# Kernel optimization log

Measured on AMD Instinct MI355X. Metric: run time of the kernel, lower is better.

## Reference

```python
import jax, jax.numpy as jnp
import numpy as np

B_PARAM = 1.0
BAND_WIDTH = 0.5
LOSS_WEIGHT = 1.0
EPS_REL = 1e-5
EPS_NORM = 1e-12


def setup_inputs() -> dict:
    key = jax.random.key(0)
    k1, k2 = jax.random.split(key)
    images = jax.random.normal(k1, (1, 256, 96, 96), dtype=jnp.float32)
    gt = jax.random.normal(k2, (1, 256, 96, 96), dtype=jnp.float32)
    return {"images": images, "gt": gt}


def _cosine_raw_distance(i_feat, t_feat):
    # _create_using_dot_p: center both by mean of t over (n, h, w), L2-normalize
    # along channels, then pairwise dot products -> cosine distance in [0, 1].
    mean_t = jnp.mean(t_feat, axis=(0, 2, 3), keepdims=True)
    i_c = i_feat - mean_t
    t_c = t_feat - mean_t
    i_n = i_c / jnp.maximum(jnp.sqrt(jnp.sum(i_c * i_c, axis=1, keepdims=True)), EPS_NORM)
    t_n = t_c / jnp.maximum(jnp.sqrt(jnp.sum(t_c * t_c, axis=1, keepdims=True)), EPS_NORM)
    n, c, h, w = i_n.shape
    t_v = t_n.reshape(n, c, h * w)
    # dot[n, h, w, s] = sum_c i_n[n,c,h,w] * t_v[n,c,s]   (the conv2d 1x1 kernel trick)
    dot = jnp.einsum('nchw,ncs->nhws', i_n, t_v)
    dist = jnp.clip((1.0 - dot) / 2.0, 0.0, None)
    return dist  # [n, h, w, h*w]


def _cx_loss(i_feat, t_feat):
    raw = _cosine_raw_distance(i_feat, t_feat)                      # [n,h,w,s]
    # relative distance (Eq. 2): divide each row by its min over target positions
    rel = raw / (jnp.min(raw, axis=-1, keepdims=True) + EPS_REL)
    w = jnp.exp((B_PARAM - rel) / BAND_WIDTH)
    cx = w / jnp.sum(w, axis=-1, keepdims=True)                     # row softmax-like
    max_gt_sim = jnp.max(cx, axis=(1, 2))                           # [n, s]
    cs = jnp.mean(max_gt_sim, axis=1)                               # [n]
    loss = jnp.mean(-jnp.log(cs))
    return loss * LOSS_WEIGHT


def reference(images, gt):
    # use_vgg=False, crop_quarter=False, h*w <= max_1d_size**2 -> direct CX loss.
    return _cx_loss(images, gt)
```

## Files before the change

kernel.cpp:

```cpp
#include <hip/hip_runtime.h>
#include <hip/hip_bf16.h>

#define S 9216
#define C 256
#define NCT 12
#define NG  (NCT*8)
#define SCH 1152

typedef __bf16 bf16x8 __attribute__((ext_vector_type(8)));
typedef float f32x4 __attribute__((ext_vector_type(4)));
typedef unsigned short us8 __attribute__((ext_vector_type(8)));
typedef unsigned short us4 __attribute__((ext_vector_type(4)));

#define GLOAD_LDS16(g, l) __builtin_amdgcn_global_load_lds( \
    (const __attribute__((address_space(1))) void*)(g),     \
    (__attribute__((address_space(3))) void*)(l), 16, 0, 0)

#define A2C 2.8853900817779268f

__device__ __forceinline__ float bf2f(unsigned short u) {
    return __uint_as_float(((unsigned)u) << 16);
}
__device__ __forceinline__ unsigned short f2bfbits(float x) {
    __hip_bfloat16 h = __float2bfloat16(x);
    return *reinterpret_cast<unsigned short*>(&h);
}

__global__ __launch_bounds__(256) void k_mean(const float* __restrict__ gt,
                                              float* __restrict__ meanT) {
    const int c = blockIdx.x;
    const float* p = gt + (size_t)c * S;
    float s = 0.f;
    for (int i = threadIdx.x; i < S; i += 256) s += p[i];
    for (int m = 1; m < 64; m <<= 1) s += __shfl_xor(s, m, 64);
    __shared__ float red[4];
    if ((threadIdx.x & 63) == 0) red[threadIdx.x >> 6] = s;
    __syncthreads();
    if (threadIdx.x == 0)
        meanT[c] = (red[0] + red[1] + red[2] + red[3]) * (1.0f / S);
}

__global__ __launch_bounds__(256) void k_ssq(const float* __restrict__ img,
                                             const float* __restrict__ gt,
                                             const float* __restrict__ meanT,
                                             float* __restrict__ ssqP) {
    __shared__ float sm[32];
    const int part = blockIdx.x & 7;
    const int sb   = blockIdx.x >> 3;
    const int t    = threadIdx.x;
    if (t < 32) sm[t] = meanT[part * 32 + t];
    __syncthreads();
    const int s = sb * 256 + t;
    float si = 0.f, st = 0.f;
    #pragma unroll 8
    for (int k = 0; k < 32; ++k) {
        const int c = part * 32 + k;
        const float m  = sm[k];
        const float di = img[(size_t)c * S + s] - m;
        const float dt = gt [(size_t)c * S + s] - m;
        si += di * di;
        st += dt * dt;
    }
    ssqP[(size_t)part * S + s]       = si;
    ssqP[(size_t)(part + 8) * S + s] = st;
}

__global__ __launch_bounds__(256) void k_write(const float* __restrict__ img,
                                               const float* __restrict__ gt,
                                               const float* __restrict__ meanT,
                                               const float* __restrict__ ssqP,
                                               __hip_bfloat16* __restrict__ A,
                                               __hip_bfloat16* __restrict__ B) {
    __shared__ float sm[32];
    const int part = blockIdx.x & 7;
    const int sb   = blockIdx.x >> 3;
    const int t    = threadIdx.x;
    if (t < 32) sm[t] = meanT[part * 32 + t];
    __syncthreads();
    const int s = sb * 256 + t;
    float si = 0.f, st = 0.f;
    #pragma unroll
    for (int p = 0; p < 8; ++p) {
        si += ssqP[(size_t)p * S + s];
        st += ssqP[(size_t)(p + 8) * S + s];
    }
    const float ri = 1.0f / fmaxf(sqrtf(si), 1e-12f);
    const float rt = 1.0f / fmaxf(sqrtf(st), 1e-12f);
    const int c0 = part * 32;
    #pragma unroll
    for (int cc = 0; cc < 4; ++cc) {
        us8 va, vb;
        #pragma unroll
        for (int e = 0; e < 8; ++e) {
            const int c = c0 + cc * 8 + e;
            const float m = sm[cc * 8 + e];
            va[e] = f2bfbits((img[(size_t)c * S + s] - m) * ri);
            vb[e] = f2bfbits((gt [(size_t)c * S + s] - m) * rt);
        }
        *reinterpret_cast<us8*>(A + (size_t)s * C + c0 + cc * 8) = va;
        *reinterpret_cast<us8*>(B + (size_t)s * C + c0 + cc * 8) = vb;
    }
}

__global__ __launch_bounds__(256) void k_init(float* __restrict__ rowmin,
                                              float* __restrict__ rowsum,
                                              float* __restrict__ colmaxLog) {
    const int i = blockIdx.x * 256 + threadIdx.x;
    if (i < S) {
        rowmin[i]     = __uint_as_float(0x7f800000u);
        rowsum[i]     = 0.f;
        colmaxLog[i]  = 0.f;
    }
}

__global__ __launch_bounds__(256, 2) void k_gemm_store(const __hip_bfloat16* __restrict__ A,
                                                       const __hip_bfloat16* __restrict__ B,
                                                       float* __restrict__ rowmin,
                                                       __hip_bfloat16* __restrict__ Q) {
    __shared__ alignas(16) __hip_bfloat16 As[64 * 256];
    __shared__ alignas(16) __hip_bfloat16 Bs[2 * 256 * 32];
    const int tid  = threadIdx.x;
    const int lane = tid & 63;
    const int wid  = tid >> 6;
    const int orig = blockIdx.x;
    const int wg   = (orig & 7) * 54 + (orig >> 3);
    const int rowBase = (wg / 3) * 64;
    const int cb0     = (wg % 3) * 3072;

    const int frow = lane & 15;
    const int kgrp = lane >> 4;

    {
        const int arow_lo = lane >> 5;
        const int achunk  = lane & 31;
        #pragma unroll
        for (int j = 0; j < 8; ++j) {
            const int row = wid * 16 + j * 2 + arow_lo;
            const int cc  = achunk ^ (row & 7);
            GLOAD_LDS16(A + (size_t)(rowBase + row) * C + cc * 8,
                        &As[(wid * 16 + j * 2) * 256 + lane * 8]);
        }
    }
    const int bcol_lo = lane >> 2;
    const int bchunk  = (lane & 3) ^ ((lane >> 3) & 3);
    #pragma unroll
    for (int g = 0; g < 2; ++g) {
        const int cb = cb0 + (g >> 3) * 256;
        const int kt = g & 7;
        #pragma unroll
        for (int i = 0; i < 4; ++i) {
            const int col = wid * 16 + i * 64 + bcol_lo;
            GLOAD_LDS16(B + (size_t)(cb + col) * C + kt * 32 + bchunk * 8,
                        &Bs[(g & 1) * 8192 + wid * 512 + i * 2048 + lane * 8]);
        }
    }

    const int bswz = (kgrp ^ ((frow >> 1) & 3)) * 8;

    for (int t = 0; t < NCT; ++t) {
        f32x4 acc[4][4] = {};
        #pragma unroll
        for (int kt = 0; kt < 8; ++kt) {
            const int g = t * 8 + kt;
            if (g < NG - 1) asm volatile("s_waitcnt vmcnt(4)" ::: "memory");
            else            asm volatile("s_waitcnt vmcnt(0)" ::: "memory");
            __builtin_amdgcn_s_barrier();

            bf16x8 af[4], bfr[4];
            #pragma unroll
            for (int m = 0; m < 4; ++m) {
                const int row = m * 16 + frow;
                const int p   = (kt * 4 + kgrp) ^ (frow & 7);
                af[m] = *reinterpret_cast<const bf16x8*>(&As[row * 256 + p * 8]);
            }
            const int bbase = (g & 1) * 8192;
            #pragma unroll
            for (int n = 0; n < 4; ++n) {
                const int col = wid * 64 + n * 16 + frow;
                bfr[n] = *reinterpret_cast<const bf16x8*>(&Bs[bbase + col * 32 + bswz]);
            }
            #pragma unroll
            for (int m = 0; m < 4; ++m)
                #pragma unroll
                for (int n = 0; n < 4; ++n)
                    acc[m][n] = __builtin_amdgcn_mfma_f32_16x16x32_bf16(af[m], bfr[n], acc[m][n], 0, 0, 0);

            __builtin_amdgcn_s_barrier();

            if (g + 2 < NG) {
                const int g2 = g + 2;
                const int cb = cb0 + (g2 >> 3) * 256;
                const int k2 = g2 & 7;
                #pragma unroll
                for (int i = 0; i < 4; ++i) {
                    const int col = wid * 16 + i * 64 + bcol_lo;
                    GLOAD_LDS16(B + (size_t)(cb + col) * C + k2 * 32 + bchunk * 8,
                                &Bs[(g2 & 1) * 8192 + wid * 512 + i * 2048 + lane * 8]);
                }
            }
        }

        const int colBase = cb0 + t * 256;
        float vmin[4][4];
        #pragma unroll
        for (int m = 0; m < 4; ++m)
            #pragma unroll
            for (int q = 0; q < 4; ++q) vmin[m][q] = 1e30f;

        #pragma unroll
        for (int n = 0; n < 4; ++n) {
            const int cg = colBase + wid * 64 + n * 16 + frow;
            #pragma unroll
            for (int m = 0; m < 4; ++m) {
                us4 pk;
                #pragma unroll
                for (int q = 0; q < 4; ++q) {
                    const float raw = fmaxf(0.5f * (1.0f - acc[m][n][q]), 0.0f);
                    vmin[m][q] = fminf(vmin[m][q], raw);
                    pk[q] = f2bfbits(raw);
                }
                *reinterpret_cast<us4*>(Q + (size_t)cg * S + rowBase + m * 16 + kgrp * 4) = pk;
            }
        }
        #pragma unroll
        for (int m = 0; m < 4; ++m)
            #pragma unroll
            for (int q = 0; q < 4; ++q) {
                float v = vmin[m][q];
                v = fminf(v, __shfl_xor(v, 1, 64));
                v = fminf(v, __shfl_xor(v, 2, 64));
                v = fminf(v, __shfl_xor(v, 4, 64));
                v = fminf(v, __shfl_xor(v, 8, 64));
                if (frow == 0)
                    atomicMin((unsigned int*)&rowmin[rowBase + m * 16 + kgrp * 4 + q],
                              __float_as_uint(v));
            }
    }
}

__global__ __launch_bounds__(256) void k_rowsum(const __hip_bfloat16* __restrict__ Q,
                                                const float* __restrict__ rowmin,
                                                float* __restrict__ rowsum) {
    __shared__ float sBrN[64];
    __shared__ float srs[64];
    const int t  = threadIdx.x;
    const int r0 = (blockIdx.x >> 3) * 64;
    const int s0 = (blockIdx.x & 7) * SCH;
    if (t < 64) {
        sBrN[t] = -A2C / (rowmin[r0 + t] + 1e-5f);
        srs[t]  = 0.f;
    }
    __syncthreads();
    const int roct = (t & 7) * 8;
    const int ss   = t >> 3;
    float brn[8];
    #pragma unroll
    for (int j = 0; j < 8; ++j) brn[j] = sBrN[roct + j];
    const __hip_bfloat16* base = Q + r0 + roct;

    float sums[8] = {};
    #pragma unroll 4
    for (int i = 0; i < SCH / 32; ++i) {
        const int s = s0 + ss + i * 32;
        const us8 v = *reinterpret_cast<const us8*>(base + (size_t)s * S);
        #pragma unroll
        for (int j = 0; j < 8; ++j)
            sums[j] += exp2f(fmaf(brn[j], bf2f(v[j]), A2C));
    }
    #pragma unroll
    for (int j = 0; j < 8; ++j) {
        float x = sums[j];
        x += __shfl_xor(x, 8, 64);
        x += __shfl_xor(x, 16, 64);
        x += __shfl_xor(x, 32, 64);
        if ((t & 63) < 8) atomicAdd(&srs[roct + j], x);
    }
    __syncthreads();
    if (t < 64) atomicAdd(&rowsum[r0 + t], srs[t]);
}

__global__ __launch_bounds__(256) void k_colmax(const __hip_bfloat16* __restrict__ Q,
                                                const float* __restrict__ rowmin,
                                                const float* __restrict__ rowsum,
                                                float* __restrict__ colmaxLog) {
    __shared__ float sBrN[64];
    __shared__ float sCA[64];
    const int t  = threadIdx.x;
    const int r0 = (blockIdx.x >> 3) * 64;
    const int s0 = (blockIdx.x & 7) * SCH;
    if (t < 64) {
        sBrN[t] = -A2C / (rowmin[r0 + t] + 1e-5f);
        sCA[t]  = A2C + 64.0f - __log2f(rowsum[r0 + t]);
    }
    __syncthreads();
    const int roct = (t & 7) * 8;
    const int ss   = t >> 3;
    float brn[8], ca[8];
    #pragma unroll
    for (int j = 0; j < 8; ++j) { brn[j] = sBrN[roct + j]; ca[j] = sCA[roct + j]; }
    const __hip_bfloat16* base = Q + r0 + roct;

    #pragma unroll 4
    for (int i = 0; i < SCH / 32; ++i) {
        const int s = s0 + ss + i * 32;
        const us8 v = *reinterpret_cast<const us8*>(base + (size_t)s * S);
        float mx = -1e30f;
        #pragma unroll
        for (int j = 0; j < 8; ++j)
            mx = fmaxf(mx, fmaf(brn[j], bf2f(v[j]), ca[j]));
        mx = fmaxf(mx, __shfl_xor(mx, 1, 64));
        mx = fmaxf(mx, __shfl_xor(mx, 2, 64));
        mx = fmaxf(mx, __shfl_xor(mx, 4, 64));
        if ((t & 7) == 0)
            atomicMax((unsigned int*)&colmaxLog[s], __float_as_uint(fmaxf(mx, 0.0f)));
    }
}

__global__ __launch_bounds__(256) void k_final(const float* __restrict__ colmaxLog,
                                               float* __restrict__ out) {
    float s = 0.f;
    for (int i = threadIdx.x; i < S; i += 256) s += exp2f(colmaxLog[i]);
    for (int m = 1; m < 64; m <<= 1) s += __shfl_xor(s, m, 64);
    __shared__ float red[4];
    if ((threadIdx.x & 63) == 0) red[threadIdx.x >> 6] = s;
    __syncthreads();
    if (threadIdx.x == 0) {
        const float total = red[0] + red[1] + red[2] + red[3];
        out[0] = -logf(total * (5.421010862427522e-20f / (float)S));
    }
}

extern "C" void kernel_launch(void* const* d_in, const int* in_sizes, int n_in,
                              void* d_out, int out_size, void* d_ws, size_t ws_size,
                              hipStream_t stream) {
    const float* img = (const float*)d_in[0];
    const float* gt  = (const float*)d_in[1];

    float* ws        = (float*)d_ws;
    float* meanT     = ws;
    float* rowmin    = ws + 256;
    float* rowsum    = rowmin + S;
    float* colmaxLog = rowsum + S;
    __hip_bfloat16* A = (__hip_bfloat16*)(colmaxLog + S);
    __hip_bfloat16* B = A + (size_t)S * C;
    __hip_bfloat16* Q = B + (size_t)S * C;
    float* ssqP = (float*)Q;
    float* out = (float*)d_out;

    k_mean <<<C, 256, 0, stream>>>(gt, meanT);
    k_ssq  <<<288, 256, 0, stream>>>(img, gt, meanT, ssqP);
    k_init <<<(S + 255) / 256, 256, 0, stream>>>(rowmin, rowsum, colmaxLog);
    k_write<<<288, 256, 0, stream>>>(img, gt, meanT, ssqP, A, B);

    k_gemm_store<<<432, 256, 0, stream>>>(A, B, rowmin, Q);
    k_rowsum<<<1152, 256, 0, stream>>>(Q, rowmin, rowsum);
    k_colmax<<<1152, 256, 0, stream>>>(Q, rowmin, rowsum, colmaxLog);

    k_final<<<1, 256, 0, stream>>>(colmaxLog, out);
}
```

Before: 247.8 us.

## Drop LDS staging in GEMM, keep A in registers, load B directly

The GEMM kernel no longer stages A and B through shared memory with async global-to-LDS loads and barriers. Each wave now holds its 64x256 A strip fragments in registers and reads B fragments straight from global memory (relying on L2). The grid doubles to 864 blocks, each covering half as many column tiles, and blocks are remapped so strips are grouped per XCD for L2 locality. This removes barrier and LDS overhead but adds register pressure from the 32 A vectors and more redundant global traffic for B, with no explicit prefetch pipelining.

```diff
diff --git a/kernel.cpp b/kernel.cpp
--- a/kernel.cpp
+++ b/kernel.cpp
@@ -3,18 +3,13 @@
 
 #define S 9216
 #define C 256
-#define NCT 12
-#define NG  (NCT*8)
+#define NCT 6
 #define SCH 1152
 
 typedef __bf16 bf16x8 __attribute__((ext_vector_type(8)));
 typedef float f32x4 __attribute__((ext_vector_type(4)));
 typedef unsigned short us8 __attribute__((ext_vector_type(8)));
 typedef unsigned short us4 __attribute__((ext_vector_type(4)));
-
-#define GLOAD_LDS16(g, l) __builtin_amdgcn_global_load_lds( \
-    (const __attribute__((address_space(1))) void*)(g),     \
-    (__attribute__((address_space(3))) void*)(l), 16, 0, 0)
 
 #define A2C 2.8853900817779268f
 
@@ -117,107 +112,63 @@
                                                        const __hip_bfloat16* __restrict__ B,
                                                        float* __restrict__ rowmin,
                                                        __hip_bfloat16* __restrict__ Q) {
-    __shared__ alignas(16) __hip_bfloat16 As[64 * 256];
-    __shared__ alignas(16) __hip_bfloat16 Bs[2 * 256 * 32];
-    const int tid  = threadIdx.x;
-    const int lane = tid & 63;
-    const int wid  = tid >> 6;
+    const int lane = threadIdx.x & 63;
+    const int wid  = threadIdx.x >> 6;
     const int orig = blockIdx.x;
-    const int wg   = (orig & 7) * 54 + (orig >> 3);
-    const int rowBase = (wg / 3) * 64;
-    const int cb0     = (wg % 3) * 3072;
+    const int xcd  = orig & 7;
+    const int q    = orig >> 3;
+    const int colGroup = q / 18;
+    const int strip    = xcd * 18 + (q % 18);
+    const int rowBase = strip * 64;
+    const int cb0     = colGroup * 1536;
 
     const int frow = lane & 15;
     const int kgrp = lane >> 4;
 
-    {
-        const int arow_lo = lane >> 5;
-        const int achunk  = lane & 31;
-        #pragma unroll
-        for (int j = 0; j < 8; ++j) {
-            const int row = wid * 16 + j * 2 + arow_lo;
-            const int cc  = achunk ^ (row & 7);
-            GLOAD_LDS16(A + (size_t)(rowBase + row) * C + cc * 8,
-                        &As[(wid * 16 + j * 2) * 256 + lane * 8]);
-        }
-    }
-    const int bcol_lo = lane >> 2;
-    const int bchunk  = (lane & 3) ^ ((lane >> 3) & 3);
-    #pragma unroll
-    for (int g = 0; g < 2; ++g) {
-        const int cb = cb0 + (g >> 3) * 256;
-        const int kt = g & 7;
-        #pragma unroll
-        for (int i = 0; i < 4; ++i) {
-            const int col = wid * 16 + i * 64 + bcol_lo;
-            GLOAD_LDS16(B + (size_t)(cb + col) * C + kt * 32 + bchunk * 8,
-                        &Bs[(g & 1) * 8192 + wid * 512 + i * 2048 + lane * 8]);
-        }
-    }
-
-    const int bswz = (kgrp ^ ((frow >> 1) & 3)) * 8;
+    bf16x8 a[4][8];
+    #pragma unroll
+    for (int m = 0; m < 4; ++m) {
+        const __hip_bfloat16* ap = A + (size_t)(rowBase + m * 16 + frow) * C + kgrp * 8;
+        #pragma unroll
+        for (int kt = 0; kt < 8; ++kt)
+            a[m][kt] = *reinterpret_cast<const bf16x8*>(ap + kt * 32);
+    }
 
     for (int t = 0; t < NCT; ++t) {
+        const int colBase = cb0 + t * 256 + wid * 64;
+        const __hip_bfloat16* bp = B + (size_t)(colBase + frow) * C + kgrp * 8;
+
         f32x4 acc[4][4] = {};
         #pragma unroll
         for (int kt = 0; kt < 8; ++kt) {
-            const int g = t * 8 + kt;
-            if (g < NG - 1) asm volatile("s_waitcnt vmcnt(4)" ::: "memory");
-            else            asm volatile("s_waitcnt vmcnt(0)" ::: "memory");
-            __builtin_amdgcn_s_barrier();
-
-            bf16x8 af[4], bfr[4];
-            #pragma unroll
-            for (int m = 0; m < 4; ++m) {
-                const int row = m * 16 + frow;
-                const int p   = (kt * 4 + kgrp) ^ (frow & 7);
-                af[m] = *reinterpret_cast<const bf16x8*>(&As[row * 256 + p * 8]);
-            }
-            const int bbase = (g & 1) * 8192;
-            #pragma unroll
-            for (int n = 0; n < 4; ++n) {
-                const int col = wid * 64 + n * 16 + frow;
-                bfr[n] = *reinterpret_cast<const bf16x8*>(&Bs[bbase + col * 32 + bswz]);
-            }
+            bf16x8 bfr[4];
+            #pragma unroll
+            for (int n = 0; n < 4; ++n)
+                bfr[n] = *reinterpret_cast<const bf16x8*>(bp + (size_t)(n * 16) * C + kt * 32);
             #pragma unroll
             for (int m = 0; m < 4; ++m)
                 #pragma unroll
                 for (int n = 0; n < 4; ++n)
-                    acc[m][n] = __builtin_amdgcn_mfma_f32_16x16x32_bf16(af[m], bfr[n], acc[m][n], 0, 0, 0);
-
-            __builtin_amdgcn_s_barrier();
-
-            if (g + 2 < NG) {
-                const int g2 = g + 2;
-                const int cb = cb0 + (g2 >> 3) * 256;
-                const int k2 = g2 & 7;
-                #pragma unroll
-                for (int i = 0; i < 4; ++i) {
-                    const int col = wid * 16 + i * 64 + bcol_lo;
-                    GLOAD_LDS16(B + (size_t)(cb + col) * C + k2 * 32 + bchunk * 8,
-                                &Bs[(g2 & 1) * 8192 + wid * 512 + i * 2048 + lane * 8]);
-                }
-            }
+                    acc[m][n] = __builtin_amdgcn_mfma_f32_16x16x32_bf16(a[m][kt], bfr[n], acc[m][n], 0, 0, 0);
         }
 
-        const int colBase = cb0 + t * 256;
         float vmin[4][4];
         #pragma unroll
         for (int m = 0; m < 4; ++m)
             #pragma unroll
-            for (int q = 0; q < 4; ++q) vmin[m][q] = 1e30f;
+            for (int qq = 0; qq < 4; ++qq) vmin[m][qq] = 1e30f;
 
         #pragma unroll
         for (int n = 0; n < 4; ++n) {
-            const int cg = colBase + wid * 64 + n * 16 + frow;
+            const int cg = colBase + n * 16 + frow;
             #pragma unroll
             for (int m = 0; m < 4; ++m) {
                 us4 pk;
                 #pragma unroll
-                for (int q = 0; q < 4; ++q) {
-                    const float raw = fmaxf(0.5f * (1.0f - acc[m][n][q]), 0.0f);
-                    vmin[m][q] = fminf(vmin[m][q], raw);
-                    pk[q] = f2bfbits(raw);
+                for (int qq = 0; qq < 4; ++qq) {
+                    const float raw = fmaxf(0.5f * (1.0f - acc[m][n][qq]), 0.0f);
+                    vmin[m][qq] = fminf(vmin[m][qq], raw);
+                    pk[qq] = f2bfbits(raw);
                 }
                 *reinterpret_cast<us4*>(Q + (size_t)cg * S + rowBase + m * 16 + kgrp * 4) = pk;
             }
@@ -225,14 +176,14 @@
         #pragma unroll
         for (int m = 0; m < 4; ++m)
             #pragma unroll
-            for (int q = 0; q < 4; ++q) {
-                float v = vmin[m][q];
+            for (int qq = 0; qq < 4; ++qq) {
+                float v = vmin[m][qq];
                 v = fminf(v, __shfl_xor(v, 1, 64));
                 v = fminf(v, __shfl_xor(v, 2, 64));
                 v = fminf(v, __shfl_xor(v, 4, 64));
                 v = fminf(v, __shfl_xor(v, 8, 64));
                 if (frow == 0)
-                    atomicMin((unsigned int*)&rowmin[rowBase + m * 16 + kgrp * 4 + q],
+                    atomicMin((unsigned int*)&rowmin[rowBase + m * 16 + kgrp * 4 + qq],
                               __float_as_uint(v));
             }
     }
@@ -352,7 +303,7 @@
     k_init <<<(S + 255) / 256, 256, 0, stream>>>(rowmin, rowsum, colmaxLog);
     k_write<<<288, 256, 0, stream>>>(img, gt, meanT, ssqP, A, B);
 
-    k_gemm_store<<<432, 256, 0, stream>>>(A, B, rowmin, Q);
+    k_gemm_store<<<864, 256, 0, stream>>>(A, B, rowmin, Q);
     k_rowsum<<<1152, 256, 0, stream>>>(Q, rowmin, rowsum);
     k_colmax<<<1152, 256, 0, stream>>>(Q, rowmin, rowsum, colmaxLog);
 
```

New measurement: 290.3 us. +17.1%, slower.

## Split GEMM columns into six groups, XCD-aware strips, hoist rowmin atomics, fuse init

Applied to the files above, without the earlier changes.

The GEMM grid doubles from 432 to 864 blocks by halving the column tiles per block (NCT 12→6, 1536-column groups). Row strips are now mapped so each XCD owns contiguous strips, which aims to improve L2 reuse of the A tile. The per-row min reduction and atomicMin are moved out of the column-tile loop so they run once per block, and the wait counts are relaxed at tile boundaries so loads overlap better. The separate init kernel is folded into k_ssq to save a launch. The cost is more blocks each reloading the A tile.

```diff
diff --git a/kernel.cpp b/kernel.cpp
--- a/kernel.cpp
+++ b/kernel.cpp
@@ -3,7 +3,7 @@
 
 #define S 9216
 #define C 256
-#define NCT 12
+#define NCT 6
 #define NG  (NCT*8)
 #define SCH 1152
 
@@ -43,14 +43,22 @@
 __global__ __launch_bounds__(256) void k_ssq(const float* __restrict__ img,
                                              const float* __restrict__ gt,
                                              const float* __restrict__ meanT,
-                                             float* __restrict__ ssqP) {
+                                             float* __restrict__ ssqP,
+                                             float* __restrict__ rowmin,
+                                             float* __restrict__ rowsum,
+                                             float* __restrict__ colmaxLog) {
     __shared__ float sm[32];
     const int part = blockIdx.x & 7;
     const int sb   = blockIdx.x >> 3;
     const int t    = threadIdx.x;
     if (t < 32) sm[t] = meanT[part * 32 + t];
-    __syncthreads();
     const int s = sb * 256 + t;
+    if (part == 0) {
+        rowmin[s]    = __uint_as_float(0x7f800000u);
+        rowsum[s]    = 0.f;
+        colmaxLog[s] = 0.f;
+    }
+    __syncthreads();
     float si = 0.f, st = 0.f;
     #pragma unroll 8
     for (int k = 0; k < 32; ++k) {
@@ -102,17 +110,6 @@
     }
 }
 
-__global__ __launch_bounds__(256) void k_init(float* __restrict__ rowmin,
-                                              float* __restrict__ rowsum,
-                                              float* __restrict__ colmaxLog) {
-    const int i = blockIdx.x * 256 + threadIdx.x;
-    if (i < S) {
-        rowmin[i]     = __uint_as_float(0x7f800000u);
-        rowsum[i]     = 0.f;
-        colmaxLog[i]  = 0.f;
-    }
-}
-
 __global__ __launch_bounds__(256, 2) void k_gemm_store(const __hip_bfloat16* __restrict__ A,
                                                        const __hip_bfloat16* __restrict__ B,
                                                        float* __restrict__ rowmin,
@@ -123,9 +120,12 @@
     const int lane = tid & 63;
     const int wid  = tid >> 6;
     const int orig = blockIdx.x;
-    const int wg   = (orig & 7) * 54 + (orig >> 3);
-    const int rowBase = (wg / 3) * 64;
-    const int cb0     = (wg % 3) * 3072;
+    const int xcd  = orig & 7;
+    const int q    = orig >> 3;
+    const int colGroup = q / 18;
+    const int strip    = xcd * 18 + (q % 18);
+    const int rowBase = strip * 64;
+    const int cb0     = colGroup * 1536;
 
     const int frow = lane & 15;
     const int kgrp = lane >> 4;
@@ -157,13 +157,20 @@
 
     const int bswz = (kgrp ^ ((frow >> 1) & 3)) * 8;
 
+    float vmin[4][4];
+    #pragma unroll
+    for (int m = 0; m < 4; ++m)
+        #pragma unroll
+        for (int qq = 0; qq < 4; ++qq) vmin[m][qq] = 1e30f;
+
     for (int t = 0; t < NCT; ++t) {
         f32x4 acc[4][4] = {};
         #pragma unroll
         for (int kt = 0; kt < 8; ++kt) {
             const int g = t * 8 + kt;
-            if (g < NG - 1) asm volatile("s_waitcnt vmcnt(4)" ::: "memory");
-            else            asm volatile("s_waitcnt vmcnt(0)" ::: "memory");
+            if (kt < 2 && t > 0)      asm volatile("s_waitcnt vmcnt(20)" ::: "memory");
+            else if (g < NG - 1)      asm volatile("s_waitcnt vmcnt(4)"  ::: "memory");
+            else                      asm volatile("s_waitcnt vmcnt(0)"  ::: "memory");
             __builtin_amdgcn_s_barrier();
 
             bf16x8 af[4], bfr[4];
@@ -201,12 +208,6 @@
         }
 
         const int colBase = cb0 + t * 256;
-        float vmin[4][4];
-        #pragma unroll
-        for (int m = 0; m < 4; ++m)
-            #pragma unroll
-            for (int q = 0; q < 4; ++q) vmin[m][q] = 1e30f;
-
         #pragma unroll
         for (int n = 0; n < 4; ++n) {
             const int cg = colBase + wid * 64 + n * 16 + frow;
@@ -214,28 +215,29 @@
             for (int m = 0; m < 4; ++m) {
                 us4 pk;
                 #pragma unroll
-                for (int q = 0; q < 4; ++q) {
-                    const float raw = fmaxf(0.5f * (1.0f - acc[m][n][q]), 0.0f);
-                    vmin[m][q] = fminf(vmin[m][q], raw);
-                    pk[q] = f2bfbits(raw);
+                for (int qq = 0; qq < 4; ++qq) {
+                    const float raw = fmaxf(0.5f * (1.0f - acc[m][n][qq]), 0.0f);
+                    vmin[m][qq] = fminf(vmin[m][qq], raw);
+                    pk[qq] = f2bfbits(raw);
                 }
                 *reinterpret_cast<us4*>(Q + (size_t)cg * S + rowBase + m * 16 + kgrp * 4) = pk;
             }
         }
-        #pragma unroll
-        for (int m = 0; m < 4; ++m)
-            #pragma unroll
-            for (int q = 0; q < 4; ++q) {
-                float v = vmin[m][q];
-                v = fminf(v, __shfl_xor(v, 1, 64));
-                v = fminf(v, __shfl_xor(v, 2, 64));
-                v = fminf(v, __shfl_xor(v, 4, 64));
-                v = fminf(v, __shfl_xor(v, 8, 64));
-                if (frow == 0)
-                    atomicMin((unsigned int*)&rowmin[rowBase + m * 16 + kgrp * 4 + q],
-                              __float_as_uint(v));
-            }
-    }
+    }
+
+    #pragma unroll
+    for (int m = 0; m < 4; ++m)
+        #pragma unroll
+        for (int qq = 0; qq < 4; ++qq) {
+            float v = vmin[m][qq];
+            v = fminf(v, __shfl_xor(v, 1, 64));
+            v = fminf(v, __shfl_xor(v, 2, 64));
+            v = fminf(v, __shfl_xor(v, 4, 64));
+            v = fminf(v, __shfl_xor(v, 8, 64));
+            if (frow == 0)
+                atomicMin((unsigned int*)&rowmin[rowBase + m * 16 + kgrp * 4 + qq],
+                          __float_as_uint(v));
+        }
 }
 
 __global__ __launch_bounds__(256) void k_rowsum(const __hip_bfloat16* __restrict__ Q,
@@ -348,11 +350,10 @@
     float* out = (float*)d_out;
 
     k_mean <<<C, 256, 0, stream>>>(gt, meanT);
-    k_ssq  <<<288, 256, 0, stream>>>(img, gt, meanT, ssqP);
-    k_init <<<(S + 255) / 256, 256, 0, stream>>>(rowmin, rowsum, colmaxLog);
+    k_ssq  <<<288, 256, 0, stream>>>(img, gt, meanT, ssqP, rowmin, rowsum, colmaxLog);
     k_write<<<288, 256, 0, stream>>>(img, gt, meanT, ssqP, A, B);
 
-    k_gemm_store<<<432, 256, 0, stream>>>(A, B, rowmin, Q);
+    k_gemm_store<<<864, 256, 0, stream>>>(A, B, rowmin, Q);
     k_rowsum<<<1152, 256, 0, stream>>>(Q, rowmin, rowsum);
     k_colmax<<<1152, 256, 0, stream>>>(Q, rowmin, rowsum, colmaxLog);
 
```

After: 218.9 us. 1.13x faster.
